# Kernel optimization log

Measured on AMD Instinct MI355X. Metric: run time of the kernel, lower is better.

The kernel has to match this reference:

```python
import jax, jax.numpy as jnp
import numpy as np

N = 4096
IN_FEATS = 64
HIDDEN = 128
STEPS = 3
SCALE = 3.0
LJ_EPS = 0.1
LJ_SIGMA = 3.5
LJ_MIX = 0.1  # 'auto' branch: pot = exp(-r/scale)*relu(score) + 0.1*lj
LN_EPS = 1e-5


def setup_inputs() -> dict:
    key = jax.random.key(0)
    ks = jax.random.split(key, 12)
    x = jax.random.normal(ks[0], (N, IN_FEATS), dtype=jnp.float32)
    # sparse-ish 0/1 adjacency (float, as multiplied in the torch code)
    adj = (jax.random.uniform(ks[1], (N, N)) < 0.02).astype(jnp.float32)
    # positive pairwise distances in Angstrom-like range
    dist_mat = jax.random.uniform(ks[2], (N, N), dtype=jnp.float32) * 10.0 + 0.5
    s_in = 1.0 / np.sqrt(IN_FEATS)
    s_h = 1.0 / np.sqrt(HIDDEN)
    s_2h = 1.0 / np.sqrt(2 * HIDDEN)
    params = {
        'W_in': jax.random.uniform(ks[3], (IN_FEATS, HIDDEN), minval=-s_in, maxval=s_in),
        'b_in': jnp.zeros((HIDDEN,), jnp.float32),
        'W_msg': jax.random.uniform(ks[4], (HIDDEN, HIDDEN), minval=-s_h, maxval=s_h),
        'b_msg': jnp.zeros((HIDDEN,), jnp.float32),
        'W_u1': jax.random.uniform(ks[5], (2 * HIDDEN, HIDDEN), minval=-s_2h, maxval=s_2h),
        'b_u1': jnp.zeros((HIDDEN,), jnp.float32),
        'W_u2': jax.random.uniform(ks[6], (HIDDEN, HIDDEN), minval=-s_h, maxval=s_h),
        'b_u2': jnp.zeros((HIDDEN,), jnp.float32),
        'gamma': jnp.ones((HIDDEN,), jnp.float32),
        'beta': jnp.zeros((HIDDEN,), jnp.float32),
    }
    return {'x': x, 'adj': adj, 'dist_mat': dist_mat, **params}


def _layernorm(x, gamma, beta):
    mu = jnp.mean(x, axis=-1, keepdims=True)
    var = jnp.mean(jnp.square(x - mu), axis=-1, keepdims=True)
    return (x - mu) * jax.lax.rsqrt(var + LN_EPS) * gamma + beta


def reference(x, adj, dist_mat, W_in, b_in, W_msg, b_msg, W_u1, b_u1, W_u2, b_u2, gamma, beta):
    h = x @ W_in + b_in  # (n, hidden)
    # distance-only terms are loop-invariant
    r_safe = jnp.clip(dist_mat, 1e-6, None)
    sr6 = (LJ_SIGMA / r_safe) ** 6
    lj = 4.0 * LJ_EPS * (sr6 * sr6 - sr6)          # (n, n)
    decay = jnp.exp(-dist_mat / SCALE)             # (n, n)
    pot_const = LJ_MIX * lj                        # 'auto' branch constant part
    for _ in range(STEPS):
        # torch code computes msg_lin(h) but never uses it (dead code) -> skipped
        # pot_scalar[i,j] = <h_i, h_j>, computed without (n,n,d) materialization
        pot_scalar = h @ h.T                       # (n, n)
        pot = decay * jax.nn.relu(pot_scalar) + pot_const
        # m_i = sum_j pot[i,j]*adj[i,j]*h_j == masked-weighted matmul
        m = (pot * adj) @ h                        # (n, hidden)
        concat = jnp.concatenate([h, m], axis=-1)  # (n, 2*hidden)
        delta = jax.nn.relu(concat @ W_u1 + b_u1) @ W_u2 + b_u2
        h = _layernorm(h + delta, gamma, beta)
    return h
```

## Files before the change

### kernel.cpp

```cpp
#include <hip/hip_runtime.h>
#include <hip/hip_bf16.h>

#define NN   4096
#define HID  128
#define INFE 64
#define KE   160
#define KMAX 192
#define CH   64
#define RPB  4
#define RPB8 8

typedef unsigned short u16;
typedef unsigned int   u32;

__device__ __forceinline__ float bfu(u16 u) { return __uint_as_float(((u32)u) << 16); }
__device__ __forceinline__ float bflo(u32 w){ return __uint_as_float(w << 16); }
__device__ __forceinline__ float bfhi(u32 w){ return __uint_as_float(w & 0xffff0000u); }
__device__ __forceinline__ u16 f2b(float f) { __hip_bfloat16 h = __float2bfloat16(f); return *(u16*)&h; }

__global__ __launch_bounds__(128) void k_h0(
    const float* __restrict__ x, const float* __restrict__ Win, const float* __restrict__ bin,
    float* __restrict__ hdst, u16* __restrict__ bdst)
{
    __shared__ float xl[INFE];
    const int r = blockIdx.x;
    const int d = threadIdx.x;
    if (d < INFE) xl[d] = x[(size_t)r*INFE + d];
    __syncthreads();
    float acc = bin[d];
    #pragma unroll 8
    for (int k = 0; k < INFE; ++k)
        acc = fmaf(xl[k], Win[k*HID + d], acc);
    hdst[(size_t)r*HID + d] = acc;
    bdst[(size_t)r*HID + d] = f2b(acc);
}

__global__ __launch_bounds__(256) void k_prep(
    const float* __restrict__ adj, const float* __restrict__ dist,
    float4* __restrict__ edges, int* __restrict__ nnzp,
    const float* __restrict__ x, const float* __restrict__ Win, const float* __restrict__ bin,
    float* __restrict__ hdst, u16* __restrict__ bdst)
{
    const int t = threadIdx.x;
    if (blockIdx.x < NN/2) {
        __shared__ int cnt[2];
        __shared__ int   cl[2][KE];
        __shared__ float ca[2][KE];
        const int r0 = blockIdx.x * 2;
        if (t < 2) cnt[t] = 0;
        __syncthreads();
        float4 av[2][4];
        #pragma unroll
        for (int rr = 0; rr < 2; ++rr) {
            const float4* arow = (const float4*)(adj + (size_t)(r0+rr)*NN);
            #pragma unroll
            for (int q = 0; q < 4; ++q) av[rr][q] = arow[t + 256*q];
        }
        #pragma unroll
        for (int rr = 0; rr < 2; ++rr) {
            #pragma unroll
            for (int q = 0; q < 4; ++q) {
                float a4[4] = {av[rr][q].x, av[rr][q].y, av[rr][q].z, av[rr][q].w};
                if (a4[0] != 0.f || a4[1] != 0.f || a4[2] != 0.f || a4[3] != 0.f) {
                    #pragma unroll
                    for (int u = 0; u < 4; ++u) {
                        if (a4[u] != 0.f) {
                            int pos = atomicAdd(&cnt[rr], 1);
                            if (pos < KE) { cl[rr][pos] = 4*(t + 256*q) + u; ca[rr][pos] = a4[u]; }
                        }
                    }
                }
            }
        }
        __syncthreads();
        #pragma unroll
        for (int rr = 0; rr < 2; ++rr) {
            const int n  = cnt[rr] < KE ? cnt[rr] : KE;
            const int np = (n + 31) / 32 * 32;
            float4* erow = edges + (size_t)(r0+rr)*KE;
            for (int i = n + t; i < np; i += 256)
                erow[i] = make_float4(__int_as_float(0), 0.f, 0.f, 0.f);
            const float* drow = dist + (size_t)(r0+rr)*NN;
            for (int i = t; i < n; i += 256) {
                int   c = cl[rr][i];
                float a = ca[rr][i];
                float d  = fmaxf(drow[c], 1e-6f);
                float dw1 = a * __expf(-d * (1.0f/3.0f));
                float tt = 3.5f / d, t2 = tt*tt, t6 = t2*t2*t2;
                float dw2 = a * 0.04f * (t6*t6 - t6);
                erow[i] = make_float4(__int_as_float(c), dw1, dw2, 0.f);
            }
            if (t == 0) nnzp[r0+rr] = np;
        }
    } else {
        __shared__ float xl[2][INFE];
        const int grp = t >> 7;
        const int d   = t & 127;
        const int r   = (blockIdx.x - NN/2) * 2 + grp;
        if (d < INFE) xl[grp][d] = x[(size_t)r*INFE + d];
        __syncthreads();
        float acc = bin[d];
        #pragma unroll 8
        for (int k = 0; k < INFE; ++k)
            acc = fmaf(xl[grp][k], Win[k*HID + d], acc);
        hdst[(size_t)r*HID + d] = acc;
        bdst[(size_t)r*HID + d] = f2b(acc);
    }
}

__global__ __launch_bounds__(512, 4) void k_fstep8(
    const float4* __restrict__ edges, const int* __restrict__ nnzp,
    const float* __restrict__ h, const u16* __restrict__ hb,
    const float* __restrict__ Wu1, const float* __restrict__ bu1,
    const float* __restrict__ Wu2, const float* __restrict__ bu2,
    const float* __restrict__ gam, const float* __restrict__ bet,
    float* __restrict__ hout, u16* __restrict__ bout)
{
    __shared__ __align__(16) float4 eds[RPB8][KE];
    __shared__ int npl[RPB8];
    __shared__ __align__(16) float hs[RPB8][HID];
    __shared__ __align__(16) float ms[RPB8][HID];
    __shared__ __align__(16) float h1s[RPB8][HID];
    __shared__ float hn[RPB8][HID];
    __shared__ float ps[4][RPB8][HID];
    const int t    = threadIdx.x;
    const int w    = t >> 6;
    const int lane = t & 63;
    const int ig   = lane & 15;
    const int grp  = lane >> 4;
    const int r0   = blockIdx.x * RPB8;
    const int r    = r0 + w;

    if (t < RPB8) npl[t] = nnzp[r0 + t];
    const float4 hiA = *(const float4*)(h + (size_t)r*HID + 8*ig);
    const float4 hiB = *(const float4*)(h + (size_t)r*HID + 8*ig + 4);
    if (grp == 0) {
        *(float4*)&hs[w][8*ig]     = hiA;
        *(float4*)&hs[w][8*ig + 4] = hiB;
    }
    __syncthreads();
    for (int i = t; i < RPB8*KE; i += 512) {
        int rr = i / KE, c = i - rr*KE;
        if (c < npl[rr]) eds[rr][c] = edges[(size_t)(r0+rr)*KE + c];
    }
    __syncthreads();

    const int np = npl[w];
    float macc[8];
    #pragma unroll
    for (int d = 0; d < 8; ++d) macc[d] = 0.f;
    for (int e0 = 0; e0 < np; e0 += 32) {
        float4 ed[8]; uint4 hj4[8]; float p[8];
        #pragma unroll
        for (int q = 0; q < 8; ++q) ed[q] = eds[w][e0 + grp + 4*q];
        #pragma unroll
        for (int q = 0; q < 8; ++q) {
            int c = __float_as_int(ed[q].x);
            hj4[q] = *(const uint4*)(hb + (size_t)c*HID + 8*ig);
        }
        #pragma unroll
        for (int q = 0; q < 8; ++q) {
            float j0 = bflo(hj4[q].x), j1 = bfhi(hj4[q].x);
            float j2 = bflo(hj4[q].y), j3 = bfhi(hj4[q].y);
            float j4 = bflo(hj4[q].z), j5 = bfhi(hj4[q].z);
            float j6 = bflo(hj4[q].w), j7 = bfhi(hj4[q].w);
            float pp = hiA.x*j0;
            pp = fmaf(hiA.y, j1, pp); pp = fmaf(hiA.z, j2, pp); pp = fmaf(hiA.w, j3, pp);
            pp = fmaf(hiB.x, j4, pp); pp = fmaf(hiB.y, j5, pp); pp = fmaf(hiB.z, j6, pp);
            p[q] = fmaf(hiB.w, j7, pp);
        }
        #pragma unroll
        for (int mask = 1; mask <= 8; mask <<= 1) {
            #pragma unroll
            for (int q = 0; q < 8; ++q) p[q] += __shfl_xor(p[q], mask);
        }
        #pragma unroll
        for (int q = 0; q < 8; ++q) {
            float wq = fmaf(ed[q].y, fmaxf(p[q], 0.f), ed[q].z);
            float j0 = bflo(hj4[q].x), j1 = bfhi(hj4[q].x);
            float j2 = bflo(hj4[q].y), j3 = bfhi(hj4[q].y);
            float j4 = bflo(hj4[q].z), j5 = bfhi(hj4[q].z);
            float j6 = bflo(hj4[q].w), j7 = bfhi(hj4[q].w);
            macc[0] = fmaf(wq, j0, macc[0]); macc[1] = fmaf(wq, j1, macc[1]);
            macc[2] = fmaf(wq, j2, macc[2]); macc[3] = fmaf(wq, j3, macc[3]);
            macc[4] = fmaf(wq, j4, macc[4]); macc[5] = fmaf(wq, j5, macc[5]);
            macc[6] = fmaf(wq, j6, macc[6]); macc[7] = fmaf(wq, j7, macc[7]);
        }
    }
    #pragma unroll
    for (int d = 0; d < 8; ++d) {
        macc[d] += __shfl_xor(macc[d], 16);
        macc[d] += __shfl_xor(macc[d], 32);
    }
    if (grp == 0) {
        float4 mA = make_float4(macc[0], macc[1], macc[2], macc[3]);
        float4 mB = make_float4(macc[4], macc[5], macc[6], macc[7]);
        *(float4*)&ms[w][8*ig]     = mA;
        *(float4*)&ms[w][8*ig + 4] = mB;
    }
    __syncthreads();

    {
        const int kq = t >> 7;
        const int d  = t & 127;
        const float binit = (kq == 0) ? bu1[d] : 0.f;
        float acc[RPB8];
        #pragma unroll
        for (int rr = 0; rr < RPB8; ++rr) acc[rr] = binit;
        const float (*src)[HID] = (kq < 2) ? hs : ms;
        const int kb = (kq & 1) * 64;
        const float* wp = Wu1 + (size_t)kq * 64 * HID + d;
        #pragma unroll 2
        for (int k = 0; k < 64; k += 4) {
            float w0 = wp[(k+0)*HID], w1 = wp[(k+1)*HID];
            float w2 = wp[(k+2)*HID], w3 = wp[(k+3)*HID];
            #pragma unroll
            for (int rr = 0; rr < RPB8; ++rr) {
                float4 c4 = *(const float4*)&src[rr][kb + k];
                acc[rr] = fmaf(c4.x, w0, acc[rr]);
                acc[rr] = fmaf(c4.y, w1, acc[rr]);
                acc[rr] = fmaf(c4.z, w2, acc[rr]);
                acc[rr] = fmaf(c4.w, w3, acc[rr]);
            }
        }
        #pragma unroll
        for (int rr = 0; rr < RPB8; ++rr) ps[kq][rr][d] = acc[rr];
    }
    __syncthreads();
    for (int pidx = t; pidx < RPB8*HID; pidx += 512) {
        int rr = pidx >> 7, d = pidx & 127;
        h1s[rr][d] = fmaxf(ps[0][rr][d] + ps[1][rr][d] + ps[2][rr][d] + ps[3][rr][d], 0.f);
    }
    __syncthreads();
    {
        const int kq = t >> 7;
        const int d  = t & 127;
        const float binit = (kq == 0) ? bu2[d] : 0.f;
        float acc[RPB8];
        #pragma unroll
        for (int rr = 0; rr < RPB8; ++rr) acc[rr] = binit;
        const int kb = kq * 32;
        const float* wp = Wu2 + (size_t)kq * 32 * HID + d;
        #pragma unroll 2
        for (int k = 0; k < 32; k += 4) {
            float w0 = wp[(k+0)*HID], w1 = wp[(k+1)*HID];
            float w2 = wp[(k+2)*HID], w3 = wp[(k+3)*HID];
            #pragma unroll
            for (int rr = 0; rr < RPB8; ++rr) {
                float4 c4 = *(const float4*)&h1s[rr][kb + k];
                acc[rr] = fmaf(c4.x, w0, acc[rr]);
                acc[rr] = fmaf(c4.y, w1, acc[rr]);
                acc[rr] = fmaf(c4.z, w2, acc[rr]);
                acc[rr] = fmaf(c4.w, w3, acc[rr]);
            }
        }
        #pragma unroll
        for (int rr = 0; rr < RPB8; ++rr) ps[kq][rr][d] = acc[rr];
    }
    __syncthreads();
    for (int pidx = t; pidx < RPB8*HID; pidx += 512) {
        int rr = pidx >> 7, d = pidx & 127;
        hn[rr][d] = hs[rr][d] + ps[0][rr][d] + ps[1][rr][d] + ps[2][rr][d] + ps[3][rr][d];
    }
    __syncthreads();
    {
        float v0 = hn[w][lane], v1 = hn[w][lane + 64];
        float s = v0 + v1;
        #pragma unroll
        for (int mask = 1; mask <= 32; mask <<= 1) s += __shfl_xor(s, mask);
        float mu = s * (1.0f/128.0f);
        float z0 = v0 - mu, z1 = v1 - mu;
        float vv = fmaf(z0, z0, z1*z1);
        #pragma unroll
        for (int mask = 1; mask <= 32; mask <<= 1) vv += __shfl_xor(vv, mask);
        float rstd = rsqrtf(vv * (1.0f/128.0f) + 1e-5f);
        float o0 = fmaf(z0 * rstd, gam[lane],      bet[lane]);
        float o1 = fmaf(z1 * rstd, gam[lane + 64], bet[lane + 64]);
        hout[(size_t)r*HID + lane]      = o0;
        hout[(size_t)r*HID + lane + 64] = o1;
        bout[(size_t)r*HID + lane]      = f2b(o0);
        bout[(size_t)r*HID + lane + 64] = f2b(o1);
    }
}

template<bool SB, bool DB>
__global__ __launch_bounds__(128) void k_step(
    const float* __restrict__ adj, const float* __restrict__ dist,
    const void* hsrc, void* hdst,
    const float* __restrict__ Wu1, const float* __restrict__ bu1,
    const float* __restrict__ Wu2, const float* __restrict__ bu2,
    const float* __restrict__ gam, const float* __restrict__ bet)
{
    __shared__ int   cnt4[RPB];
    __shared__ int   cl[RPB][KMAX];
    __shared__ float w1l[RPB][KMAX], w2l[RPB][KMAX];
    __shared__ __align__(16) float hs4[RPB][HID];
    __shared__ __align__(16) float hj[CH][HID + 1];
    __shared__ float pl[CH];
    __shared__ __align__(16) float ms[RPB][HID];
    __shared__ __align__(16) float h1s[RPB][HID];
    __shared__ float hn[RPB][HID];
    const int r0 = blockIdx.x * RPB;
    const int t  = threadIdx.x;
    const u16*   s16 = (const u16*)hsrc;
    const float* s32 = (const float*)hsrc;
    if (t < RPB) cnt4[t] = 0;
    for (int i = t; i < RPB*HID; i += 128) {
        int rr = i >> 7, d = i & 127;
        hs4[rr][d] = SB ? bfu(s16[(size_t)(r0+rr)*HID + d]) : s32[(size_t)(r0+rr)*HID + d];
    }
    __syncthreads();
    for (int idx = t; idx < RPB*(NN/4); idx += 128) {
        int rr = idx >> 10, c4 = idx & 1023;
        float4 a4 = ((const float4*)(adj + (size_t)(r0+rr)*NN))[c4];
        if (a4.x != 0.f || a4.y != 0.f || a4.z != 0.f || a4.w != 0.f) {
            const float* drow = dist + (size_t)(r0+rr)*NN;
            float av4[4] = {a4.x, a4.y, a4.z, a4.w};
            #pragma unroll
            for (int q = 0; q < 4; ++q) {
                float av = av4[q];
                if (av != 0.f) {
                    int c = 4*c4 + q;
                    float d  = fmaxf(drow[c], 1e-6f);
                    float dw1 = av * __expf(-d * (1.0f/3.0f));
                    float tt = 3.5f / d, t2 = tt*tt, t6 = t2*t2*t2;
                    float dw2 = av * 0.04f * (t6*t6 - t6);
                    int pos = atomicAdd(&cnt4[rr], 1);
                    if (pos < KMAX) { cl[rr][pos] = c; w1l[rr][pos] = dw1; w2l[rr][pos] = dw2; }
                }
            }
        }
    }
    __syncthreads();
    int npv[RPB];
    for (int rr = 0; rr < RPB; ++rr) {
        int n  = cnt4[rr] < KMAX ? cnt4[rr] : KMAX;
        int np = (n + CH - 1) / CH * CH;
        npv[rr] = np;
        for (int i = n + t; i < np; i += 128) { cl[rr][i] = 0; w1l[rr][i] = 0.f; w2l[rr][i] = 0.f; }
    }
    __syncthreads();
    const int e2 = t >> 1, hf = t & 1;
    for (int rr = 0; rr < RPB; ++rr) {
        float acc = 0.f;
        for (int e0 = 0; e0 < npv[rr]; e0 += CH) {
            int c = cl[rr][e0 + e2];
            float* dst = &hj[e2][hf*64];
            if (SB) {
                const uint4* sv = (const uint4*)(s16 + (size_t)c*HID + hf*64);
                #pragma unroll
                for (int i = 0; i < 8; ++i) {
                    uint4 v = sv[i];
                    dst[8*i+0] = __uint_as_float(v.x << 16); dst[8*i+1] = __uint_as_float(v.x & 0xffff0000u);
                    dst[8*i+2] = __uint_as_float(v.y << 16); dst[8*i+3] = __uint_as_float(v.y & 0xffff0000u);
                    dst[8*i+4] = __uint_as_float(v.z << 16); dst[8*i+5] = __uint_as_float(v.z & 0xffff0000u);
                    dst[8*i+6] = __uint_as_float(v.w << 16); dst[8*i+7] = __uint_as_float(v.w & 0xffff0000u);
                }
            } else {
                const float4* sv = (const float4*)(s32 + (size_t)c*HID + hf*64);
                #pragma unroll
                for (int i = 0; i < 16; ++i) {
                    float4 v = sv[i];
                    dst[4*i+0] = v.x; dst[4*i+1] = v.y; dst[4*i+2] = v.z; dst[4*i+3] = v.w;
                }
            }
            __syncthreads();
            {
                const float* ha = &hs4[rr][hf*64];
                const float* hb = &hj[e2][hf*64];
                float p = 0.f;
                #pragma unroll
                for (int i = 0; i < 64; ++i) p = fmaf(ha[i], hb[i], p);
                p += __shfl_xor(p, 1);
                if (hf == 0) pl[e2] = fmaf(w1l[rr][e0+e2], fmaxf(p, 0.f), w2l[rr][e0+e2]);
            }
            __syncthreads();
            #pragma unroll
            for (int i = 0; i < CH; ++i) acc = fmaf(pl[i], hj[i][t], acc);
            __syncthreads();
        }
        ms[rr][t] = acc;
    }
    __syncthreads();
    {
        float bb = bu1[t];
        float a0 = bb, a1 = bb, a2 = bb, a3 = bb;
        for (int k = 0; k < HID; k += 4) {
            float w0 = Wu1[(k+0)*HID + t], w1 = Wu1[(k+1)*HID + t];
            float w2 = Wu1[(k+2)*HID + t], w3 = Wu1[(k+3)*HID + t];
            float4 c0 = *(const float4*)&hs4[0][k];
            float4 c1 = *(const float4*)&hs4[1][k];
            float4 c2 = *(const float4*)&hs4[2][k];
            float4 c3 = *(const float4*)&hs4[3][k];
            a0 = fmaf(c0.x,w0,a0); a0 = fmaf(c0.y,w1,a0); a0 = fmaf(c0.z,w2,a0); a0 = fmaf(c0.w,w3,a0);
            a1 = fmaf(c1.x,w0,a1); a1 = fmaf(c1.y,w1,a1); a1 = fmaf(c1.z,w2,a1); a1 = fmaf(c1.w,w3,a1);
            a2 = fmaf(c2.x,w0,a2); a2 = fmaf(c2.y,w1,a2); a2 = fmaf(c2.z,w2,a2); a2 = fmaf(c2.w,w3,a2);
            a3 = fmaf(c3.x,w0,a3); a3 = fmaf(c3.y,w1,a3); a3 = fmaf(c3.z,w2,a3); a3 = fmaf(c3.w,w3,a3);
        }
        for (int k = 0; k < HID; k += 4) {
            float w0 = Wu1[(HID+k+0)*HID + t], w1 = Wu1[(HID+k+1)*HID + t];
            float w2 = Wu1[(HID+k+2)*HID + t], w3 = Wu1[(HID+k+3)*HID + t];
            float4 c0 = *(const float4*)&ms[0][k];
            float4 c1 = *(const float4*)&ms[1][k];
            float4 c2 = *(const float4*)&ms[2][k];
            float4 c3 = *(const float4*)&ms[3][k];
            a0 = fmaf(c0.x,w0,a0); a0 = fmaf(c0.y,w1,a0); a0 = fmaf(c0.z,w2,a0); a0 = fmaf(c0.w,w3,a0);
            a1 = fmaf(c1.x,w0,a1); a1 = fmaf(c1.y,w1,a1); a1 = fmaf(c1.z,w2,a1); a1 = fmaf(c1.w,w3,a1);
            a2 = fmaf(c2.x,w0,a2); a2 = fmaf(c2.y,w1,a2); a2 = fmaf(c2.z,w2,a2); a2 = fmaf(c2.w,w3,a2);
            a3 = fmaf(c3.x,w0,a3); a3 = fmaf(c3.y,w1,a3); a3 = fmaf(c3.z,w2,a3); a3 = fmaf(c3.w,w3,a3);
        }
        h1s[0][t] = fmaxf(a0,0.f); h1s[1][t] = fmaxf(a1,0.f);
        h1s[2][t] = fmaxf(a2,0.f); h1s[3][t] = fmaxf(a3,0.f);
    }
    __syncthreads();
    {
        float bb = bu2[t];
        float b0 = bb, b1 = bb, b2 = bb, b3 = bb;
        for (int k = 0; k < HID; k += 4) {
            float w0 = Wu2[(k+0)*HID + t], w1 = Wu2[(k+1)*HID + t];
            float w2 = Wu2[(k+2)*HID + t], w3 = Wu2[(k+3)*HID + t];
            float4 c0 = *(const float4*)&h1s[0][k];
            float4 c1 = *(const float4*)&h1s[1][k];
            float4 c2 = *(const float4*)&h1s[2][k];
            float4 c3 = *(const float4*)&h1s[3][k];
            b0 = fmaf(c0.x,w0,b0); b0 = fmaf(c0.y,w1,b0); b0 = fmaf(c0.z,w2,b0); b0 = fmaf(c0.w,w3,b0);
            b1 = fmaf(c1.x,w0,b1); b1 = fmaf(c1.y,w1,b1); b1 = fmaf(c1.z,w2,b1); b1 = fmaf(c1.w,w3,b1);
            b2 = fmaf(c2.x,w0,b2); b2 = fmaf(c2.y,w1,b2); b2 = fmaf(c2.z,w2,b2); b2 = fmaf(c2.w,w3,b2);
            b3 = fmaf(c3.x,w0,b3); b3 = fmaf(c3.y,w1,b3); b3 = fmaf(c3.z,w2,b3); b3 = fmaf(c3.w,w3,b3);
        }
        hn[0][t] = hs4[0][t] + b0; hn[1][t] = hs4[1][t] + b1;
        hn[2][t] = hs4[2][t] + b2; hn[3][t] = hs4[3][t] + b3;
    }
    __syncthreads();
    {
        const int lr = t >> 5, j = t & 31;
        float s = 0.f;
        #pragma unroll
        for (int q = 0; q < 4; ++q) s += hn[lr][j + 32*q];
        #pragma unroll
        for (int k2 = 16; k2 >= 1; k2 >>= 1) s += __shfl_xor(s, k2);
        float mu = s * (1.0f/128.0f);
        float v = 0.f;
        #pragma unroll
        for (int q = 0; q < 4; ++q) { float z = hn[lr][j + 32*q] - mu; v = fmaf(z, z, v); }
        #pragma unroll
        for (int k2 = 16; k2 >= 1; k2 >>= 1) v += __shfl_xor(v, k2);
        float rstd = rsqrtf(v * (1.0f/128.0f) + 1e-5f);
        #pragma unroll
        for (int q = 0; q < 4; ++q) {
            int dd = j + 32*q;
            float val = fmaf((hn[lr][dd] - mu) * rstd, gam[dd], bet[dd]);
            if (DB) ((u16*)hdst)[(size_t)(r0+lr)*HID + dd] = f2b(val);
            else    ((float*)hdst)[(size_t)(r0+lr)*HID + dd] = val;
        }
    }
}

extern "C" void kernel_launch(void* const* d_in, const int* in_sizes, int n_in,
                              void* d_out, int out_size, void* d_ws, size_t ws_size,
                              hipStream_t stream)
{
    const float* x    = (const float*)d_in[0];
    const float* adj  = (const float*)d_in[1];
    const float* dist = (const float*)d_in[2];
    const float* Win  = (const float*)d_in[3];
    const float* bin  = (const float*)d_in[4];
    const float* Wu1  = (const float*)d_in[7];
    const float* bu1  = (const float*)d_in[8];
    const float* Wu2  = (const float*)d_in[9];
    const float* bu2  = (const float*)d_in[10];
    const float* gam  = (const float*)d_in[11];
    const float* bet  = (const float*)d_in[12];

    const size_t ebytes = (size_t)NN * KE * sizeof(float4);
    const size_t cbytes = ((size_t)NN * sizeof(int) + 255) & ~255;
    const size_t hb32   = (size_t)NN * HID * sizeof(float);
    const size_t hb16   = (size_t)NN * HID * sizeof(u16);
    const size_t need   = ebytes + cbytes + hb32 + 2*hb16;

    if (ws_size >= need) {
        char* p = (char*)d_ws;
        float4* edges = (float4*)p;            p += ebytes;
        int*    nnzp  = (int*)p;               p += cbytes;
        float*  hA    = (float*)p;             p += hb32;
        u16*    bA    = (u16*)p;               p += hb16;
        u16*    bB    = (u16*)p;               p += hb16;
        float*  hB    = (float*)d_out;

        k_prep<<<NN, 256, 0, stream>>>(adj, dist, edges, nnzp, x, Win, bin, hA, bA);
        k_fstep8<<<NN/RPB8, 512, 0, stream>>>(edges, nnzp, hA, bA, Wu1, bu1, Wu2, bu2, gam, bet, hB, bB);
        k_fstep8<<<NN/RPB8, 512, 0, stream>>>(edges, nnzp, hB, bB, Wu1, bu1, Wu2, bu2, gam, bet, hA, bA);
        k_fstep8<<<NN/RPB8, 512, 0, stream>>>(edges, nnzp, hA, bA, Wu1, bu1, Wu2, bu2, gam, bet, hB, bB);
    } else if (ws_size >= hb32) {
        void* A = d_ws; void* B = d_out;
        k_h0<<<NN, 128, 0, stream>>>(x, Win, bin, (float*)A, (u16*)B);
        k_step<false,false><<<NN/RPB, 128, 0, stream>>>(adj, dist, A, B, Wu1, bu1, Wu2, bu2, gam, bet);
        k_step<false,false><<<NN/RPB, 128, 0, stream>>>(adj, dist, B, A, Wu1, bu1, Wu2, bu2, gam, bet);
        k_step<false,false><<<NN/RPB, 128, 0, stream>>>(adj, dist, A, B, Wu1, bu1, Wu2, bu2, gam, bet);
    }
}
```

Before: 233.7 us.

## Compact adjacency rows per wavefront with ballot/popcount and alias partial-sum LDS

The prep kernel now assigns one 64-lane wavefront per adjacency row and builds the compacted edge list with ballot plus popcount prefix sums, replacing LDS atomics, the shared staging arrays and the second pass. Edge weights are computed and written directly in the scan, and each block now handles 8 rows, with 4 rows per block on the embedding side. Because positions come from a prefix sum, edge order follows column index rather than atomic order. Separately, the step kernel reuses the edge LDS buffer for its partial-sum array to cut shared memory per block and possibly raise occupancy, which is only safe if the edges are no longer needed once partial sums are written.

```diff
diff --git a/kernel.cpp b/kernel.cpp
--- a/kernel.cpp
+++ b/kernel.cpp
@@ -35,68 +35,56 @@
     bdst[(size_t)r*HID + d] = f2b(acc);
 }
 
-__global__ __launch_bounds__(256) void k_prep(
+__global__ __launch_bounds__(512) void k_prep(
     const float* __restrict__ adj, const float* __restrict__ dist,
     float4* __restrict__ edges, int* __restrict__ nnzp,
     const float* __restrict__ x, const float* __restrict__ Win, const float* __restrict__ bin,
     float* __restrict__ hdst, u16* __restrict__ bdst)
 {
     const int t = threadIdx.x;
-    if (blockIdx.x < NN/2) {
-        __shared__ int cnt[2];
-        __shared__ int   cl[2][KE];
-        __shared__ float ca[2][KE];
-        const int r0 = blockIdx.x * 2;
-        if (t < 2) cnt[t] = 0;
-        __syncthreads();
-        float4 av[2][4];
-        #pragma unroll
-        for (int rr = 0; rr < 2; ++rr) {
-            const float4* arow = (const float4*)(adj + (size_t)(r0+rr)*NN);
-            #pragma unroll
-            for (int q = 0; q < 4; ++q) av[rr][q] = arow[t + 256*q];
-        }
-        #pragma unroll
-        for (int rr = 0; rr < 2; ++rr) {
-            #pragma unroll
-            for (int q = 0; q < 4; ++q) {
-                float a4[4] = {av[rr][q].x, av[rr][q].y, av[rr][q].z, av[rr][q].w};
-                if (a4[0] != 0.f || a4[1] != 0.f || a4[2] != 0.f || a4[3] != 0.f) {
-                    #pragma unroll
-                    for (int u = 0; u < 4; ++u) {
-                        if (a4[u] != 0.f) {
-                            int pos = atomicAdd(&cnt[rr], 1);
-                            if (pos < KE) { cl[rr][pos] = 4*(t + 256*q) + u; ca[rr][pos] = a4[u]; }
-                        }
+    if (blockIdx.x < NN/RPB8) {
+        const int w    = t >> 6;
+        const int lane = t & 63;
+        const int r    = blockIdx.x * RPB8 + w;
+        const float4* arow = (const float4*)(adj + (size_t)r*NN);
+        const float*  drow = dist + (size_t)r*NN;
+        float4*       erow = edges + (size_t)r*KE;
+        float4 av[16];
+        #pragma unroll
+        for (int q = 0; q < 16; ++q) av[q] = arow[lane + 64*q];
+        const unsigned long long below = (1ULL << lane) - 1ULL;
+        int cnt = 0;
+        #pragma unroll
+        for (int q = 0; q < 16; ++q) {
+            float a4[4] = {av[q].x, av[q].y, av[q].z, av[q].w};
+            #pragma unroll
+            for (int u = 0; u < 4; ++u) {
+                const bool hit = (a4[u] != 0.f);
+                unsigned long long m = __ballot(hit);
+                if (hit) {
+                    int pos = cnt + __popcll(m & below);
+                    if (pos < KE) {
+                        int   c = 4*(lane + 64*q) + u;
+                        float d  = fmaxf(drow[c], 1e-6f);
+                        float dw1 = a4[u] * __expf(-d * (1.0f/3.0f));
+                        float tt = 3.5f / d, t2 = tt*tt, t6 = t2*t2*t2;
+                        float dw2 = a4[u] * 0.04f * (t6*t6 - t6);
+                        erow[pos] = make_float4(__int_as_float(c), dw1, dw2, 0.f);
                     }
                 }
-            }
-        }
-        __syncthreads();
-        #pragma unroll
-        for (int rr = 0; rr < 2; ++rr) {
-            const int n  = cnt[rr] < KE ? cnt[rr] : KE;
-            const int np = (n + 31) / 32 * 32;
-            float4* erow = edges + (size_t)(r0+rr)*KE;
-            for (int i = n + t; i < np; i += 256)
-                erow[i] = make_float4(__int_as_float(0), 0.f, 0.f, 0.f);
-            const float* drow = dist + (size_t)(r0+rr)*NN;
-            for (int i = t; i < n; i += 256) {
-                int   c = cl[rr][i];
-                float a = ca[rr][i];
-                float d  = fmaxf(drow[c], 1e-6f);
-                float dw1 = a * __expf(-d * (1.0f/3.0f));
-                float tt = 3.5f / d, t2 = tt*tt, t6 = t2*t2*t2;
-                float dw2 = a * 0.04f * (t6*t6 - t6);
-                erow[i] = make_float4(__int_as_float(c), dw1, dw2, 0.f);
-            }
-            if (t == 0) nnzp[r0+rr] = np;
-        }
+                cnt += __popcll(m);
+            }
+        }
+        int n  = cnt < KE ? cnt : KE;
+        int np = (n + 31) / 32 * 32;
+        if (lane < np - n)
+            erow[n + lane] = make_float4(__int_as_float(0), 0.f, 0.f, 0.f);
+        if (lane == 0) nnzp[r] = np;
     } else {
-        __shared__ float xl[2][INFE];
+        __shared__ float xl[4][INFE];
         const int grp = t >> 7;
         const int d   = t & 127;
-        const int r   = (blockIdx.x - NN/2) * 2 + grp;
+        const int r   = (blockIdx.x - NN/RPB8) * 4 + grp;
         if (d < INFE) xl[grp][d] = x[(size_t)r*INFE + d];
         __syncthreads();
         float acc = bin[d];
@@ -122,7 +110,7 @@
     __shared__ __align__(16) float ms[RPB8][HID];
     __shared__ __align__(16) float h1s[RPB8][HID];
     __shared__ float hn[RPB8][HID];
-    __shared__ float ps[4][RPB8][HID];
+    float (*ps)[RPB8][HID] = reinterpret_cast<float(*)[RPB8][HID]>(&eds[0][0]);
     const int t    = threadIdx.x;
     const int w    = t >> 6;
     const int lane = t & 63;
@@ -487,7 +475,7 @@
         u16*    bB    = (u16*)p;               p += hb16;
         float*  hB    = (float*)d_out;
 
-        k_prep<<<NN, 256, 0, stream>>>(adj, dist, edges, nnzp, x, Win, bin, hA, bA);
+        k_prep<<<NN/RPB8 + NN/4, 512, 0, stream>>>(adj, dist, edges, nnzp, x, Win, bin, hA, bA);
         k_fstep8<<<NN/RPB8, 512, 0, stream>>>(edges, nnzp, hA, bA, Wu1, bu1, Wu2, bu2, gam, bet, hB, bB);
         k_fstep8<<<NN/RPB8, 512, 0, stream>>>(edges, nnzp, hB, bB, Wu1, bu1, Wu2, bu2, gam, bet, hA, bA);
         k_fstep8<<<NN/RPB8, 512, 0, stream>>>(edges, nnzp, hA, bA, Wu1, bu1, Wu2, bu2, gam, bet, hB, bB);
```

After: 254.9 us. +9.1%, slower.

## Read edges directly from global, use DPP reductions, split MLP K eight ways

Applied to the files above, without the earlier changes.

The step kernel stops staging each row's edge list in shared memory. Each wave now reads its edges straight from global memory, which removes the staging loop and one block-wide barrier. The 16-lane dot-product reduction uses DPP row operations instead of xor shuffles. The two MLP matmuls are re-tiled so each wave covers a smaller K slice across all 128 outputs, with an eight-way partial-sum reduction in shared memory in place of four-way. Each thread holds twice as many accumulators, so register pressure rises, and edge loads lose the coalescing the shared-memory staging provided.

```diff
diff --git a/kernel.cpp b/kernel.cpp
--- a/kernel.cpp
+++ b/kernel.cpp
@@ -17,6 +17,12 @@
 __device__ __forceinline__ float bflo(u32 w){ return __uint_as_float(w << 16); }
 __device__ __forceinline__ float bfhi(u32 w){ return __uint_as_float(w & 0xffff0000u); }
 __device__ __forceinline__ u16 f2b(float f) { __hip_bfloat16 h = __float2bfloat16(f); return *(u16*)&h; }
+
+template<int CTRL>
+__device__ __forceinline__ float dppadd(float v) {
+    return v + __uint_as_float((u32)__builtin_amdgcn_update_dpp(
+        0, (int)__float_as_uint(v), CTRL, 0xF, 0xF, true));
+}
 
 __global__ __launch_bounds__(128) void k_h0(
     const float* __restrict__ x, const float* __restrict__ Win, const float* __restrict__ bin,
@@ -116,13 +122,11 @@
     const float* __restrict__ gam, const float* __restrict__ bet,
     float* __restrict__ hout, u16* __restrict__ bout)
 {
-    __shared__ __align__(16) float4 eds[RPB8][KE];
-    __shared__ int npl[RPB8];
+    __shared__ __align__(16) float ps[8][RPB8][HID];
     __shared__ __align__(16) float hs[RPB8][HID];
     __shared__ __align__(16) float ms[RPB8][HID];
     __shared__ __align__(16) float h1s[RPB8][HID];
     __shared__ float hn[RPB8][HID];
-    __shared__ float ps[4][RPB8][HID];
     const int t    = threadIdx.x;
     const int w    = t >> 6;
     const int lane = t & 63;
@@ -131,28 +135,22 @@
     const int r0   = blockIdx.x * RPB8;
     const int r    = r0 + w;
 
-    if (t < RPB8) npl[t] = nnzp[r0 + t];
+    const int np = nnzp[r];
     const float4 hiA = *(const float4*)(h + (size_t)r*HID + 8*ig);
     const float4 hiB = *(const float4*)(h + (size_t)r*HID + 8*ig + 4);
     if (grp == 0) {
         *(float4*)&hs[w][8*ig]     = hiA;
         *(float4*)&hs[w][8*ig + 4] = hiB;
     }
-    __syncthreads();
-    for (int i = t; i < RPB8*KE; i += 512) {
-        int rr = i / KE, c = i - rr*KE;
-        if (c < npl[rr]) eds[rr][c] = edges[(size_t)(r0+rr)*KE + c];
-    }
-    __syncthreads();
-
-    const int np = npl[w];
+
+    const float4* erow = edges + (size_t)r*KE;
     float macc[8];
     #pragma unroll
     for (int d = 0; d < 8; ++d) macc[d] = 0.f;
     for (int e0 = 0; e0 < np; e0 += 32) {
         float4 ed[8]; uint4 hj4[8]; float p[8];
         #pragma unroll
-        for (int q = 0; q < 8; ++q) ed[q] = eds[w][e0 + grp + 4*q];
+        for (int q = 0; q < 8; ++q) ed[q] = erow[e0 + grp + 4*q];
         #pragma unroll
         for (int q = 0; q < 8; ++q) {
             int c = __float_as_int(ed[q].x);
@@ -170,9 +168,11 @@
             p[q] = fmaf(hiB.w, j7, pp);
         }
         #pragma unroll
-        for (int mask = 1; mask <= 8; mask <<= 1) {
-            #pragma unroll
-            for (int q = 0; q < 8; ++q) p[q] += __shfl_xor(p[q], mask);
+        for (int q = 0; q < 8; ++q) {
+            p[q] = dppadd<0x128>(p[q]);
+            p[q] = dppadd<0x124>(p[q]);
+            p[q] = dppadd<0x122>(p[q]);
+            p[q] = dppadd<0x121>(p[q]);
         }
         #pragma unroll
         for (int q = 0; q < 8; ++q) {
@@ -193,74 +193,88 @@
         macc[d] += __shfl_xor(macc[d], 32);
     }
     if (grp == 0) {
-        float4 mA = make_float4(macc[0], macc[1], macc[2], macc[3]);
-        float4 mB = make_float4(macc[4], macc[5], macc[6], macc[7]);
-        *(float4*)&ms[w][8*ig]     = mA;
-        *(float4*)&ms[w][8*ig + 4] = mB;
+        *(float4*)&ms[w][8*ig]     = make_float4(macc[0], macc[1], macc[2], macc[3]);
+        *(float4*)&ms[w][8*ig + 4] = make_float4(macc[4], macc[5], macc[6], macc[7]);
     }
     __syncthreads();
 
     {
-        const int kq = t >> 7;
-        const int d  = t & 127;
-        const float binit = (kq == 0) ? bu1[d] : 0.f;
-        float acc[RPB8];
-        #pragma unroll
-        for (int rr = 0; rr < RPB8; ++rr) acc[rr] = binit;
-        const float (*src)[HID] = (kq < 2) ? hs : ms;
-        const int kb = (kq & 1) * 64;
-        const float* wp = Wu1 + (size_t)kq * 64 * HID + d;
+        const int kq = t >> 6;
+        const int dd = t & 63;
+        const float bi0 = (kq == 0) ? bu1[dd]      : 0.f;
+        const float bi1 = (kq == 0) ? bu1[dd + 64] : 0.f;
+        float a0[RPB8], a1[RPB8];
+        #pragma unroll
+        for (int rr = 0; rr < RPB8; ++rr) { a0[rr] = bi0; a1[rr] = bi1; }
+        const float (*src)[HID] = (kq < 4) ? hs : ms;
+        const int kb = (kq & 3) * 32;
+        const float* wp = Wu1 + (size_t)(kq * 32) * HID + dd;
         #pragma unroll 2
-        for (int k = 0; k < 64; k += 4) {
-            float w0 = wp[(k+0)*HID], w1 = wp[(k+1)*HID];
-            float w2 = wp[(k+2)*HID], w3 = wp[(k+3)*HID];
+        for (int k = 0; k < 32; k += 4) {
+            float w00 = wp[(k+0)*HID], w01 = wp[(k+0)*HID + 64];
+            float w10 = wp[(k+1)*HID], w11 = wp[(k+1)*HID + 64];
+            float w20 = wp[(k+2)*HID], w21 = wp[(k+2)*HID + 64];
+            float w30 = wp[(k+3)*HID], w31 = wp[(k+3)*HID + 64];
             #pragma unroll
             for (int rr = 0; rr < RPB8; ++rr) {
                 float4 c4 = *(const float4*)&src[rr][kb + k];
-                acc[rr] = fmaf(c4.x, w0, acc[rr]);
-                acc[rr] = fmaf(c4.y, w1, acc[rr]);
-                acc[rr] = fmaf(c4.z, w2, acc[rr]);
-                acc[rr] = fmaf(c4.w, w3, acc[rr]);
-            }
-        }
-        #pragma unroll
-        for (int rr = 0; rr < RPB8; ++rr) ps[kq][rr][d] = acc[rr];
+                a0[rr] = fmaf(c4.x, w00, a0[rr]); a0[rr] = fmaf(c4.y, w10, a0[rr]);
+                a0[rr] = fmaf(c4.z, w20, a0[rr]); a0[rr] = fmaf(c4.w, w30, a0[rr]);
+                a1[rr] = fmaf(c4.x, w01, a1[rr]); a1[rr] = fmaf(c4.y, w11, a1[rr]);
+                a1[rr] = fmaf(c4.z, w21, a1[rr]); a1[rr] = fmaf(c4.w, w31, a1[rr]);
+            }
+        }
+        #pragma unroll
+        for (int rr = 0; rr < RPB8; ++rr) {
+            ps[kq][rr][dd]      = a0[rr];
+            ps[kq][rr][dd + 64] = a1[rr];
+        }
     }
     __syncthreads();
     for (int pidx = t; pidx < RPB8*HID; pidx += 512) {
         int rr = pidx >> 7, d = pidx & 127;
-        h1s[rr][d] = fmaxf(ps[0][rr][d] + ps[1][rr][d] + ps[2][rr][d] + ps[3][rr][d], 0.f);
+        float s = ps[0][rr][d] + ps[1][rr][d] + ps[2][rr][d] + ps[3][rr][d]
+                + ps[4][rr][d] + ps[5][rr][d] + ps[6][rr][d] + ps[7][rr][d];
+        h1s[rr][d] = fmaxf(s, 0.f);
     }
     __syncthreads();
     {
-        const int kq = t >> 7;
-        const int d  = t & 127;
-        const float binit = (kq == 0) ? bu2[d] : 0.f;
-        float acc[RPB8];
-        #pragma unroll
-        for (int rr = 0; rr < RPB8; ++rr) acc[rr] = binit;
-        const int kb = kq * 32;
-        const float* wp = Wu2 + (size_t)kq * 32 * HID + d;
-        #pragma unroll 2
-        for (int k = 0; k < 32; k += 4) {
-            float w0 = wp[(k+0)*HID], w1 = wp[(k+1)*HID];
-            float w2 = wp[(k+2)*HID], w3 = wp[(k+3)*HID];
+        const int kq = t >> 6;
+        const int dd = t & 63;
+        const float bi0 = (kq == 0) ? bu2[dd]      : 0.f;
+        const float bi1 = (kq == 0) ? bu2[dd + 64] : 0.f;
+        float a0[RPB8], a1[RPB8];
+        #pragma unroll
+        for (int rr = 0; rr < RPB8; ++rr) { a0[rr] = bi0; a1[rr] = bi1; }
+        const int kb = kq * 16;
+        const float* wp = Wu2 + (size_t)(kq * 16) * HID + dd;
+        #pragma unroll
+        for (int k = 0; k < 16; k += 4) {
+            float w00 = wp[(k+0)*HID], w01 = wp[(k+0)*HID + 64];
+            float w10 = wp[(k+1)*HID], w11 = wp[(k+1)*HID + 64];
+            float w20 = wp[(k+2)*HID], w21 = wp[(k+2)*HID + 64];
+            float w30 = wp[(k+3)*HID], w31 = wp[(k+3)*HID + 64];
             #pragma unroll
             for (int rr = 0; rr < RPB8; ++rr) {
                 float4 c4 = *(const float4*)&h1s[rr][kb + k];
-                acc[rr] = fmaf(c4.x, w0, acc[rr]);
-                acc[rr] = fmaf(c4.y, w1, acc[rr]);
-                acc[rr] = fmaf(c4.z, w2, acc[rr]);
-                acc[rr] = fmaf(c4.w, w3, acc[rr]);
-            }
-        }
-        #pragma unroll
-        for (int rr = 0; rr < RPB8; ++rr) ps[kq][rr][d] = acc[rr];
+                a0[rr] = fmaf(c4.x, w00, a0[rr]); a0[rr] = fmaf(c4.y, w10, a0[rr]);
+                a0[rr] = fmaf(c4.z, w20, a0[rr]); a0[rr] = fmaf(c4.w, w30, a0[rr]);
+                a1[rr] = fmaf(c4.x, w01, a1[rr]); a1[rr] = fmaf(c4.y, w11, a1[rr]);
+                a1[rr] = fmaf(c4.z, w21, a1[rr]); a1[rr] = fmaf(c4.w, w31, a1[rr]);
+            }
+        }
+        #pragma unroll
+        for (int rr = 0; rr < RPB8; ++rr) {
+            ps[kq][rr][dd]      = a0[rr];
+            ps[kq][rr][dd + 64] = a1[rr];
+        }
     }
     __syncthreads();
     for (int pidx = t; pidx < RPB8*HID; pidx += 512) {
         int rr = pidx >> 7, d = pidx & 127;
-        hn[rr][d] = hs[rr][d] + ps[0][rr][d] + ps[1][rr][d] + ps[2][rr][d] + ps[3][rr][d];
+        hn[rr][d] = hs[rr][d]
+                  + ps[0][rr][d] + ps[1][rr][d] + ps[2][rr][d] + ps[3][rr][d]
+                  + ps[4][rr][d] + ps[5][rr][d] + ps[6][rr][d] + ps[7][rr][d];
     }
     __syncthreads();
     {
@@ -487,7 +501,7 @@
         u16*    bB    = (u16*)p;               p += hb16;
         float*  hB    = (float*)d_out;
 
-        k_prep<<<NN, 256, 0, stream>>>(adj, dist, edges, nnzp, x, Win, bin, hA, bA);
+        k_prep<<<NN/2 + NN/2, 256, 0, stream>>>(adj, dist, edges, nnzp, x, Win, bin, hA, bA);
         k_fstep8<<<NN/RPB8, 512, 0, stream>>>(edges, nnzp, hA, bA, Wu1, bu1, Wu2, bu2, gam, bet, hB, bB);
         k_fstep8<<<NN/RPB8, 512, 0, stream>>>(edges, nnzp, hB, bB, Wu1, bu1, Wu2, bu2, gam, bet, hA, bA);
         k_fstep8<<<NN/RPB8, 512, 0, stream>>>(edges, nnzp, hA, bA, Wu1, bu1, Wu2, bu2, gam, bet, hB, bB);
```

New measurement: 224.8 us. 1.04x faster.
